# Kernel tuning notes

Hardware: AMD Instinct MI355X
Metric: run time of the kernel (lower is better)

## Reference

```python
import jax, jax.numpy as jnp
import numpy as np

D_MODEL = 1024
N_HEADS = 16
D_K = D_MODEL // N_HEADS
D_HIDDEN = 2048
LN_EPS = 1e-5


def setup_inputs() -> dict:
    key = jax.random.key(0)
    ks = jax.random.split(key, 16)
    s = 0.02
    inp = {
        'x': jax.random.normal(ks[0], (4, 2048, D_MODEL), dtype=jnp.float32),
        'Wq': jax.random.normal(ks[1], (D_MODEL, D_MODEL), dtype=jnp.float32) * s,
        'bq': jnp.zeros((D_MODEL,), jnp.float32),
        'Wk': jax.random.normal(ks[2], (D_MODEL, D_MODEL), dtype=jnp.float32) * s,
        'bk': jnp.zeros((D_MODEL,), jnp.float32),
        'Wv': jax.random.normal(ks[3], (D_MODEL, D_MODEL), dtype=jnp.float32) * s,
        'bv': jnp.zeros((D_MODEL,), jnp.float32),
        'Wo': jax.random.normal(ks[4], (D_MODEL, D_MODEL), dtype=jnp.float32) * s,
        'bo': jnp.zeros((D_MODEL,), jnp.float32),
        'ln1_g': jnp.ones((D_MODEL,), jnp.float32),
        'ln1_b': jnp.zeros((D_MODEL,), jnp.float32),
        'ln2_g': jnp.ones((D_MODEL,), jnp.float32),
        'ln2_b': jnp.zeros((D_MODEL,), jnp.float32),
        'W1': jax.random.normal(ks[5], (2 * D_HIDDEN, D_MODEL), dtype=jnp.float32) * s,
        'b1': jnp.zeros((2 * D_HIDDEN,), jnp.float32),
        'W2': jax.random.normal(ks[6], (D_MODEL, D_HIDDEN), dtype=jnp.float32) * s,
        'b2': jnp.zeros((D_MODEL,), jnp.float32),
    }
    return inp


def _layernorm(x, g, b):
    mu = jnp.mean(x, axis=-1, keepdims=True)
    var = jnp.mean(jnp.square(x - mu), axis=-1, keepdims=True)
    return (x - mu) * jax.lax.rsqrt(var + LN_EPS) * g + b


def _attention(xn, Wq, bq, Wk, bk, Wv, bv, Wo, bo):
    B, S, _ = xn.shape
    def split_heads(t):  # [B,S,D] -> [B,H,S,Dk]
        return t.reshape(B, S, N_HEADS, D_K).transpose(0, 2, 1, 3)
    Q = split_heads(xn @ Wq.T + bq)
    K = split_heads(xn @ Wk.T + bk)
    V = split_heads(xn @ Wv.T + bv)
    scores = jnp.einsum('bhqd,bhkd->bhqk', Q, K) / jnp.float32(D_K ** 0.5)
    attn = jax.nn.softmax(scores, axis=-1)  # torch code does max-sub + softmax (same math)
    ctx = jnp.einsum('bhqk,bhkd->bhqd', attn, V)
    ctx = ctx.transpose(0, 2, 1, 3).reshape(B, S, D_MODEL)
    return ctx @ Wo.T + bo


def reference(x, Wq, bq, Wk, bk, Wv, bv, Wo, bo, ln1_g, ln1_b, ln2_g, ln2_b, W1, b1, W2, b2):
    # pre-norm attention block
    xn = _layernorm(x, ln1_g, ln1_b)
    x = x + _attention(xn, Wq, bq, Wk, bk, Wv, bv, Wo, bo)
    # pre-norm ReGLU FFN
    xn = _layernorm(x, ln2_g, ln2_b)
    h = xn @ W1.T + b1
    a, b_ = jnp.split(h, 2, axis=-1)
    h = jax.nn.relu(a) * b_
    x = x + (h @ W2.T + b2)
    return x
```

## Files before the change

kernel.cpp:

```cpp
#include <hip/hip_runtime.h>
#include <hip/hip_bf16.h>

typedef __attribute__((ext_vector_type(8))) short short8;
typedef __attribute__((ext_vector_type(4))) float floatx4;

#define LN_EPS 1e-5f
#define EXP2_SCALE 0.18033688011112042f

__device__ __forceinline__ float b2f(unsigned short u) {
    union { float f; unsigned int i; } x; x.i = ((unsigned int)u) << 16; return x.f;
}
__device__ __forceinline__ unsigned short f2b(float f) {
    union { float f; unsigned int i; } x; x.f = f;
    unsigned int r = x.i + 0x7fffu + ((x.i >> 16) & 1u);
    return (unsigned short)(r >> 16);
}
__device__ __forceinline__ unsigned short f2b_trunc(float f) {
    union { float f; unsigned int i; } x; x.f = f;
    return (unsigned short)(x.i >> 16);
}

__device__ __forceinline__ void async16(const unsigned short* g, unsigned short* l) {
    __builtin_amdgcn_global_load_lds(
        (const __attribute__((address_space(1))) unsigned int*)g,
        (__attribute__((address_space(3))) unsigned int*)l, 16, 0, 0);
}

__global__ __launch_bounds__(256)
void cvt_all(const float* __restrict__ Wq, const float* __restrict__ Wk,
             const float* __restrict__ Wv, const float* __restrict__ Wo,
             const float* __restrict__ W1, const float* __restrict__ W2,
             unsigned short* __restrict__ dst)
{
    const size_t i = (size_t)(blockIdx.x * 256 + threadIdx.x) * 8;
    const float* src; size_t off;
    if (i < 4194304) {
        int w = (int)(i >> 20);
        src = (w == 0) ? Wq : (w == 1) ? Wk : (w == 2) ? Wv : Wo;
        off = i & 1048575;
    } else if (i < 8388608) { src = W1; off = i - 4194304; }
    else                    { src = W2; off = i - 8388608; }
    float4 a = *reinterpret_cast<const float4*>(src + off);
    float4 b = *reinterpret_cast<const float4*>(src + off + 4);
    short8 r;
    r[0] = (short)f2b(a.x); r[1] = (short)f2b(a.y);
    r[2] = (short)f2b(a.z); r[3] = (short)f2b(a.w);
    r[4] = (short)f2b(b.x); r[5] = (short)f2b(b.y);
    r[6] = (short)f2b(b.z); r[7] = (short)f2b(b.w);
    *reinterpret_cast<short8*>(dst + i) = r;
}

__global__ __launch_bounds__(256)
void ln_kernel(const float* __restrict__ x, const float* __restrict__ g,
               const float* __restrict__ bb, unsigned short* __restrict__ out)
{
    __shared__ float red[8];
    const int row = blockIdx.x, tid = threadIdx.x;
    const float* xr = x + (size_t)row * 1024;
    float v[4];
#pragma unroll
    for (int i = 0; i < 4; i++) v[i] = xr[tid + i * 256];
    float s  = v[0] + v[1] + v[2] + v[3];
    float sq = v[0]*v[0] + v[1]*v[1] + v[2]*v[2] + v[3]*v[3];
#pragma unroll
    for (int o = 32; o >= 1; o >>= 1) {
        s  += __shfl_xor(s,  o, 64);
        sq += __shfl_xor(sq, o, 64);
    }
    const int wave = tid >> 6, lane = tid & 63;
    if (lane == 0) { red[wave] = s; red[4 + wave] = sq; }
    __syncthreads();
    s  = red[0] + red[1] + red[2] + red[3];
    sq = red[4] + red[5] + red[6] + red[7];
    const float mu  = s * (1.0f / 1024.0f);
    const float var = sq * (1.0f / 1024.0f) - mu * mu;
    const float rs  = rsqrtf(var + LN_EPS);
#pragma unroll
    for (int i = 0; i < 4; i++) {
        int c = tid + i * 256;
        float o = (v[i] - mu) * rs * g[c] + bb[c];
        out[(size_t)row * 1024 + c] = f2b(o);
    }
}

struct GemmFrag {
    floatx4 acc[4][4];
};

template<int EPI>
__global__ __launch_bounds__(256, 2)
void gemm_nt(const unsigned short* __restrict__ A, const unsigned short* __restrict__ B,
             const float* __restrict__ bias, const float* __restrict__ res,
             void* __restrict__ C, int M, int N, int K)
{
    __shared__ unsigned short As[128 * 32];
    __shared__ unsigned short Bs[128 * 32];
    const int m0 = blockIdx.y * 128, n0 = blockIdx.x * 128;
    const int tid = threadIdx.x, wave = tid >> 6, lane = tid & 63;
    const int wm = (wave >> 1) * 64, wn = (wave & 1) * 64;
    const int lrow = lane & 15, quad = lane >> 4;
    const int srow = wave * 32 + (lane >> 2);
    const int scol = (lane & 3) * 8;

    floatx4 acc[4][4] = {};
    const unsigned short* gA = A + (size_t)(m0 + srow) * K + scol;
    const unsigned short* gB = B + (size_t)(n0 + srow) * K + scol;
    unsigned short* lA = &As[(wave * 32) * 32];
    unsigned short* lB = &Bs[(wave * 32) * 32];

    for (int k0 = 0; k0 < K; k0 += 32) {
        __syncthreads();
        async16(gA + k0, lA);
        async16(gA + k0 + (size_t)16 * K, lA + 16 * 32);
        async16(gB + k0, lB);
        async16(gB + k0 + (size_t)16 * K, lB + 16 * 32);
        __syncthreads();
        short8 af[4], bf[4];
#pragma unroll
        for (int i = 0; i < 4; i++)
            af[i] = *reinterpret_cast<const short8*>(&As[(wm + i * 16 + lrow) * 32 + quad * 8]);
#pragma unroll
        for (int j = 0; j < 4; j++)
            bf[j] = *reinterpret_cast<const short8*>(&Bs[(wn + j * 16 + lrow) * 32 + quad * 8]);
#pragma unroll
        for (int i = 0; i < 4; i++)
#pragma unroll
            for (int j = 0; j < 4; j++)
                acc[i][j] = __builtin_amdgcn_mfma_f32_16x16x32_bf16(af[i], bf[j], acc[i][j], 0, 0, 0);
    }

#pragma unroll
    for (int i = 0; i < 4; i++) {
        int rb = m0 + wm + i * 16 + quad * 4;
#pragma unroll
        for (int j = 0; j < 4; j++) {
            int col = n0 + wn + j * 16 + lrow;
            float bv = bias[col];
            if (EPI == 2) {
                int b = rb >> 11, spos = rb & 2047;
                int h = col >> 6, d = col & 63;
                unsigned short* dst = (unsigned short*)C +
                    (((size_t)(b * 16 + h) * 64 + d) << 11) + spos;
                unsigned int u01 = (unsigned int)f2b(acc[i][j][0] + bv) |
                                   ((unsigned int)f2b(acc[i][j][1] + bv) << 16);
                unsigned int u23 = (unsigned int)f2b(acc[i][j][2] + bv) |
                                   ((unsigned int)f2b(acc[i][j][3] + bv) << 16);
                *reinterpret_cast<uint2*>(dst) = make_uint2(u01, u23);
            } else {
#pragma unroll
                for (int r = 0; r < 4; r++) {
                    size_t idx = (size_t)(rb + r) * N + col;
                    float v = acc[i][j][r] + bv;
                    if (EPI == 0) ((unsigned short*)C)[idx] = f2b(v);
                    else          ((float*)C)[idx] = v + res[idx];
                }
            }
        }
    }
}

__global__ __launch_bounds__(256, 2)
void gemm_qkv(const unsigned short* __restrict__ A, const unsigned short* __restrict__ Wqkv,
              const float* __restrict__ bq, const float* __restrict__ bk, const float* __restrict__ bv,
              unsigned short* __restrict__ QK, unsigned short* __restrict__ Vt)
{
    __shared__ unsigned short As[128 * 32];
    __shared__ unsigned short Bs[128 * 32];
    const int part = blockIdx.x >> 3;
    const int m0 = blockIdx.y * 128, n0 = (blockIdx.x & 7) * 128;
    const int tid = threadIdx.x, wave = tid >> 6, lane = tid & 63;
    const int wm = (wave >> 1) * 64, wn = (wave & 1) * 64;
    const int lrow = lane & 15, quad = lane >> 4;
    const int srow = wave * 32 + (lane >> 2);
    const int scol = (lane & 3) * 8;
    const unsigned short* B = Wqkv + (size_t)part * 1048576;
    const float* bias = (part == 0) ? bq : (part == 1) ? bk : bv;

    floatx4 acc[4][4] = {};
    const unsigned short* gA = A + (size_t)(m0 + srow) * 1024 + scol;
    const unsigned short* gB = B + (size_t)(n0 + srow) * 1024 + scol;
    unsigned short* lA = &As[(wave * 32) * 32];
    unsigned short* lB = &Bs[(wave * 32) * 32];

    for (int k0 = 0; k0 < 1024; k0 += 32) {
        __syncthreads();
        async16(gA + k0, lA);
        async16(gA + k0 + (size_t)16 * 1024, lA + 16 * 32);
        async16(gB + k0, lB);
        async16(gB + k0 + (size_t)16 * 1024, lB + 16 * 32);
        __syncthreads();
        short8 af[4], bf[4];
#pragma unroll
        for (int i = 0; i < 4; i++)
            af[i] = *reinterpret_cast<const short8*>(&As[(wm + i * 16 + lrow) * 32 + quad * 8]);
#pragma unroll
        for (int j = 0; j < 4; j++)
            bf[j] = *reinterpret_cast<const short8*>(&Bs[(wn + j * 16 + lrow) * 32 + quad * 8]);
#pragma unroll
        for (int i = 0; i < 4; i++)
#pragma unroll
            for (int j = 0; j < 4; j++)
                acc[i][j] = __builtin_amdgcn_mfma_f32_16x16x32_bf16(af[i], bf[j], acc[i][j], 0, 0, 0);
    }

#pragma unroll
    for (int i = 0; i < 4; i++) {
        int rb = m0 + wm + i * 16 + quad * 4;
#pragma unroll
        for (int j = 0; j < 4; j++) {
            int col = n0 + wn + j * 16 + lrow;
            float bv2 = bias[col];
            if (part < 2) {
                unsigned short* dst = QK + (size_t)part * 8388608;
#pragma unroll
                for (int r = 0; r < 4; r++)
                    dst[(size_t)(rb + r) * 1024 + col] = f2b(acc[i][j][r] + bv2);
            } else {
                int b = rb >> 11, spos = rb & 2047;
                int h = col >> 6, d = col & 63;
                unsigned short* dst = Vt + (((size_t)(b * 16 + h) * 64 + d) << 11) + spos;
                unsigned int u01 = (unsigned int)f2b(acc[i][j][0] + bv2) |
                                   ((unsigned int)f2b(acc[i][j][1] + bv2) << 16);
                unsigned int u23 = (unsigned int)f2b(acc[i][j][2] + bv2) |
                                   ((unsigned int)f2b(acc[i][j][3] + bv2) << 16);
                *reinterpret_cast<uint2*>(dst) = make_uint2(u01, u23);
            }
        }
    }
}

__global__ __launch_bounds__(256, 2)
void gemm_w1_reglu(const unsigned short* __restrict__ A, const unsigned short* __restrict__ B,
                   const float* __restrict__ bias, unsigned short* __restrict__ G)
{
    __shared__ unsigned short As[128 * 32];
    __shared__ unsigned short B0s[128 * 32];
    __shared__ unsigned short B1s[128 * 32];
    const int m0 = blockIdx.y * 128, n0 = blockIdx.x * 128;
    const int tid = threadIdx.x, wave = tid >> 6, lane = tid & 63;
    const int wm = (wave >> 1) * 64, wn = (wave & 1) * 64;
    const int lrow = lane & 15, quad = lane >> 4;
    const int srow = wave * 32 + (lane >> 2);
    const int scol = (lane & 3) * 8;

    floatx4 acca[4][4] = {};
    floatx4 accb[4][4] = {};
    const unsigned short* gA  = A + (size_t)(m0 + srow) * 1024 + scol;
    const unsigned short* gB0 = B + (size_t)(n0 + srow) * 1024 + scol;
    const unsigned short* gB1 = B + (size_t)(2048 + n0 + srow) * 1024 + scol;
    unsigned short* lA  = &As [(wave * 32) * 32];
    unsigned short* lB0 = &B0s[(wave * 32) * 32];
    unsigned short* lB1 = &B1s[(wave * 32) * 32];

    for (int k0 = 0; k0 < 1024; k0 += 32) {
        __syncthreads();
        async16(gA  + k0, lA);
        async16(gA  + k0 + (size_t)16 * 1024, lA  + 16 * 32);
        async16(gB0 + k0, lB0);
        async16(gB0 + k0 + (size_t)16 * 1024, lB0 + 16 * 32);
        async16(gB1 + k0, lB1);
        async16(gB1 + k0 + (size_t)16 * 1024, lB1 + 16 * 32);
        __syncthreads();
        short8 af[4], b0[4], b1[4];
#pragma unroll
        for (int i = 0; i < 4; i++)
            af[i] = *reinterpret_cast<const short8*>(&As[(wm + i * 16 + lrow) * 32 + quad * 8]);
#pragma unroll
        for (int j = 0; j < 4; j++) {
            b0[j] = *reinterpret_cast<const short8*>(&B0s[(wn + j * 16 + lrow) * 32 + quad * 8]);
            b1[j] = *reinterpret_cast<const short8*>(&B1s[(wn + j * 16 + lrow) * 32 + quad * 8]);
        }
#pragma unroll
        for (int i = 0; i < 4; i++)
#pragma unroll
            for (int j = 0; j < 4; j++) {
                acca[i][j] = __builtin_amdgcn_mfma_f32_16x16x32_bf16(af[i], b0[j], acca[i][j], 0, 0, 0);
                accb[i][j] = __builtin_amdgcn_mfma_f32_16x16x32_bf16(af[i], b1[j], accb[i][j], 0, 0, 0);
            }
    }

#pragma unroll
    for (int i = 0; i < 4; i++) {
        int rb = m0 + wm + i * 16 + quad * 4;
#pragma unroll
        for (int j = 0; j < 4; j++) {
            int col = n0 + wn + j * 16 + lrow;
            float ba = bias[col], bb2 = bias[2048 + col];
#pragma unroll
            for (int r = 0; r < 4; r++) {
                float va = acca[i][j][r] + ba;
                float vb = accb[i][j][r] + bb2;
                G[(size_t)(rb + r) * 2048 + col] = f2b(fmaxf(va, 0.0f) * vb);
            }
        }
    }
}

__global__ __launch_bounds__(256, 2)
void attn_kernel(const unsigned short* __restrict__ Qm, const unsigned short* __restrict__ Km,
                 const unsigned short* __restrict__ Vt, unsigned short* __restrict__ ctx)
{
    __shared__ unsigned short Ks[64][72];
    __shared__ unsigned short Vs[64][72];
    __shared__ unsigned short Ps[4][32][72];

    const int tid = threadIdx.x, wave = tid >> 6, lane = tid & 63;
    const int lrow = lane & 15, quad = lane >> 4;
    const int qb = blockIdx.x, bh = blockIdx.y;
    const size_t base  = (size_t)(bh >> 4) * 2048 * 1024 + (size_t)(bh & 15) * 64;
    const size_t vbase = (size_t)bh * 131072;
    const int q0 = qb * 128 + wave * 32;

    short8 qf[2][2];
#pragma unroll
    for (int m = 0; m < 2; m++) {
        const unsigned short* qp = Qm + base + (size_t)(q0 + m * 16 + lrow) * 1024 + quad * 8;
        qf[m][0] = *reinterpret_cast<const short8*>(qp);
        qf[m][1] = *reinterpret_cast<const short8*>(qp + 32);
    }

    floatx4 o[2][4] = {};
    float li[2][4] = {};

    const int c0 = tid, c1 = tid + 256;
    for (int t = 0; t < 32; t++) {
        const int k0 = t * 64;
        __syncthreads();
        {
            int r0 = c0 >> 3, col0 = (c0 & 7) << 3;
            int r1 = c1 >> 3, col1 = (c1 & 7) << 3;
            *reinterpret_cast<uint4*>(&Ks[r0][col0]) =
                *reinterpret_cast<const uint4*>(Km + base + (size_t)(k0 + r0) * 1024 + col0);
            *reinterpret_cast<uint4*>(&Ks[r1][col1]) =
                *reinterpret_cast<const uint4*>(Km + base + (size_t)(k0 + r1) * 1024 + col1);
            *reinterpret_cast<uint4*>(&Vs[r0][col0]) =
                *reinterpret_cast<const uint4*>(Vt + vbase + (size_t)r0 * 2048 + k0 + col0);
            *reinterpret_cast<uint4*>(&Vs[r1][col1]) =
                *reinterpret_cast<const uint4*>(Vt + vbase + (size_t)r1 * 2048 + k0 + col1);
        }
        __syncthreads();

        short8 kf0[4], kf1[4];
#pragma unroll
        for (int j = 0; j < 4; j++) {
            kf0[j] = *reinterpret_cast<const short8*>(&Ks[j * 16 + lrow][quad * 8]);
            kf1[j] = *reinterpret_cast<const short8*>(&Ks[j * 16 + lrow][32 + quad * 8]);
        }
        floatx4 s4[2][4] = {};
#pragma unroll
        for (int m = 0; m < 2; m++)
#pragma unroll
            for (int j = 0; j < 4; j++) {
                s4[m][j] = __builtin_amdgcn_mfma_f32_16x16x32_bf16(qf[m][0], kf0[j], s4[m][j], 0, 0, 0);
                s4[m][j] = __builtin_amdgcn_mfma_f32_16x16x32_bf16(qf[m][1], kf1[j], s4[m][j], 0, 0, 0);
            }

#pragma unroll
        for (int m = 0; m < 2; m++)
#pragma unroll
            for (int r = 0; r < 4; r++) {
                float acc = 0.f;
#pragma unroll
                for (int j = 0; j < 4; j++) {
                    float p = __builtin_amdgcn_exp2f(s4[m][j][r] * EXP2_SCALE);
                    acc += p;
                    Ps[wave][m * 16 + quad * 4 + r][j * 16 + lrow] = f2b_trunc(p);
                }
                li[m][r] += acc;
            }
        __asm__ volatile("s_waitcnt lgkmcnt(0)" ::: "memory");

        short8 pf[2][2];
#pragma unroll
        for (int m = 0; m < 2; m++) {
            pf[m][0] = *reinterpret_cast<const short8*>(&Ps[wave][m * 16 + lrow][quad * 8]);
            pf[m][1] = *reinterpret_cast<const short8*>(&Ps[wave][m * 16 + lrow][32 + quad * 8]);
        }
#pragma unroll
        for (int jj = 0; jj < 4; jj++) {
            short8 vf0 = *reinterpret_cast<const short8*>(&Vs[jj * 16 + lrow][quad * 8]);
            short8 vf1 = *reinterpret_cast<const short8*>(&Vs[jj * 16 + lrow][32 + quad * 8]);
#pragma unroll
            for (int m = 0; m < 2; m++) {
                o[m][jj] = __builtin_amdgcn_mfma_f32_16x16x32_bf16(pf[m][0], vf0, o[m][jj], 0, 0, 0);
                o[m][jj] = __builtin_amdgcn_mfma_f32_16x16x32_bf16(pf[m][1], vf1, o[m][jj], 0, 0, 0);
            }
        }
    }

#pragma unroll
    for (int m = 0; m < 2; m++)
#pragma unroll
        for (int r = 0; r < 4; r++) {
            float l = li[m][r];
            l += __shfl_xor(l, 1, 64);
            l += __shfl_xor(l, 2, 64);
            l += __shfl_xor(l, 4, 64);
            l += __shfl_xor(l, 8, 64);
            float inv = 1.0f / l;
            int srow = q0 + m * 16 + quad * 4 + r;
#pragma unroll
            for (int jj = 0; jj < 4; jj++)
                ctx[base + (size_t)srow * 1024 + jj * 16 + lrow] = f2b(o[m][jj][r] * inv);
        }
}

extern "C" void kernel_launch(void* const* d_in, const int* in_sizes, int n_in,
                              void* d_out, int out_size, void* d_ws, size_t ws_size,
                              hipStream_t stream) {
    const float* x    = (const float*)d_in[0];
    const float* Wq   = (const float*)d_in[1];
    const float* bq   = (const float*)d_in[2];
    const float* Wk   = (const float*)d_in[3];
    const float* bk   = (const float*)d_in[4];
    const float* Wv   = (const float*)d_in[5];
    const float* bv   = (const float*)d_in[6];
    const float* Wo   = (const float*)d_in[7];
    const float* bo   = (const float*)d_in[8];
    const float* ln1g = (const float*)d_in[9];
    const float* ln1b = (const float*)d_in[10];
    const float* ln2g = (const float*)d_in[11];
    const float* ln2b = (const float*)d_in[12];
    const float* W1   = (const float*)d_in[13];
    const float* b1   = (const float*)d_in[14];
    const float* W2   = (const float*)d_in[15];
    const float* b2   = (const float*)d_in[16];
    float* out = (float*)d_out;

    char* ws = (char*)d_ws;
    unsigned short* wflat = (unsigned short*)ws;
    unsigned short* wqb = wflat;
    unsigned short* wob = wflat + 3145728;
    unsigned short* w1b = wflat + 4194304;
    unsigned short* w2b = wflat + 8388608;
    unsigned short* xn  = (unsigned short*)(ws + 20971520);
    unsigned short* Qm  = (unsigned short*)(ws + 37748736);
    unsigned short* Vt  = (unsigned short*)(ws + 71303168);
    float*          x1  = (float*)(ws + 37748736);
    unsigned short* g   = (unsigned short*)(ws + 71303168);

    dim3 blk(256);
    cvt_all<<<5120, blk, 0, stream>>>(Wq, Wk, Wv, Wo, W1, W2, wflat);
    ln_kernel<<<8192, blk, 0, stream>>>(x, ln1g, ln1b, xn);
    gemm_qkv<<<dim3(24, 64), blk, 0, stream>>>(xn, wqb, bq, bk, bv, Qm, Vt);
    attn_kernel<<<dim3(16, 64), blk, 0, stream>>>(Qm, Qm + 8388608, Vt, xn);
    gemm_nt<1><<<dim3(8, 64), blk, 0, stream>>>(xn, wob, bo, x, x1, 8192, 1024, 1024);
    ln_kernel<<<8192, blk, 0, stream>>>(x1, ln2g, ln2b, xn);
    gemm_w1_reglu<<<dim3(16, 64), blk, 0, stream>>>(xn, w1b, b1, g);
    gemm_nt<1><<<dim3(8, 64), blk, 0, stream>>>(g, w2b, b2, x1, out, 8192, 1024, 2048);
}
```

Baseline: 494.9 us.

## Widen GEMM K-tile to 64 with XOR-swizzled LDS and async attention loads

All GEMM kernels now stage 64-wide K slices in LDS, with an XOR swizzle on both the global-to-LDS copy and the fragment reads, halving the number of barrier pairs per K loop and avoiding bank conflicts. The attention kernel switches its K/V staging from register round-trip copies to direct global-to-LDS async loads using the same swizzle. The softmax exp2 scale is folded into the Q projection epilogue, which removes a multiply per score. Launch bounds are raised to 3 blocks per CU, at the cost of doubled LDS per block and tighter register limits that could cause spills.

```diff
diff --git a/kernel.cpp b/kernel.cpp
--- a/kernel.cpp
+++ b/kernel.cpp
@@ -83,45 +83,55 @@
     }
 }
 
-struct GemmFrag {
-    floatx4 acc[4][4];
-};
-
 template<int EPI>
-__global__ __launch_bounds__(256, 2)
+__global__ __launch_bounds__(256, 3)
 void gemm_nt(const unsigned short* __restrict__ A, const unsigned short* __restrict__ B,
              const float* __restrict__ bias, const float* __restrict__ res,
              void* __restrict__ C, int M, int N, int K)
 {
-    __shared__ unsigned short As[128 * 32];
-    __shared__ unsigned short Bs[128 * 32];
+    __shared__ unsigned short As[128 * 64];
+    __shared__ unsigned short Bs[128 * 64];
     const int m0 = blockIdx.y * 128, n0 = blockIdx.x * 128;
     const int tid = threadIdx.x, wave = tid >> 6, lane = tid & 63;
     const int wm = (wave >> 1) * 64, wn = (wave & 1) * 64;
     const int lrow = lane & 15, quad = lane >> 4;
-    const int srow = wave * 32 + (lane >> 2);
-    const int scol = (lane & 3) * 8;
+    const int srow = wave * 32 + (lane >> 3);
+    const int scol = (((lane & 7) ^ ((lane >> 3) & 7)) << 3);
+    const int ca0 = (quad ^ (lrow & 7)) << 3;
+    const int ca1 = ((quad + 4) ^ (lrow & 7)) << 3;
 
     floatx4 acc[4][4] = {};
     const unsigned short* gA = A + (size_t)(m0 + srow) * K + scol;
     const unsigned short* gB = B + (size_t)(n0 + srow) * K + scol;
-    unsigned short* lA = &As[(wave * 32) * 32];
-    unsigned short* lB = &Bs[(wave * 32) * 32];
-
-    for (int k0 = 0; k0 < K; k0 += 32) {
-        __syncthreads();
-        async16(gA + k0, lA);
-        async16(gA + k0 + (size_t)16 * K, lA + 16 * 32);
-        async16(gB + k0, lB);
-        async16(gB + k0 + (size_t)16 * K, lB + 16 * 32);
+    unsigned short* lA = &As[(wave * 32) * 64];
+    unsigned short* lB = &Bs[(wave * 32) * 64];
+
+    for (int k0 = 0; k0 < K; k0 += 64) {
+        __syncthreads();
+#pragma unroll
+        for (int r = 0; r < 4; r++) {
+            async16(gA + k0 + (size_t)(r * 8) * K, lA + r * 8 * 64);
+            async16(gB + k0 + (size_t)(r * 8) * K, lB + r * 8 * 64);
+        }
         __syncthreads();
         short8 af[4], bf[4];
 #pragma unroll
         for (int i = 0; i < 4; i++)
-            af[i] = *reinterpret_cast<const short8*>(&As[(wm + i * 16 + lrow) * 32 + quad * 8]);
+            af[i] = *reinterpret_cast<const short8*>(&As[(wm + i * 16 + lrow) * 64 + ca0]);
 #pragma unroll
         for (int j = 0; j < 4; j++)
-            bf[j] = *reinterpret_cast<const short8*>(&Bs[(wn + j * 16 + lrow) * 32 + quad * 8]);
+            bf[j] = *reinterpret_cast<const short8*>(&Bs[(wn + j * 16 + lrow) * 64 + ca0]);
+#pragma unroll
+        for (int i = 0; i < 4; i++)
+#pragma unroll
+            for (int j = 0; j < 4; j++)
+                acc[i][j] = __builtin_amdgcn_mfma_f32_16x16x32_bf16(af[i], bf[j], acc[i][j], 0, 0, 0);
+#pragma unroll
+        for (int i = 0; i < 4; i++)
+            af[i] = *reinterpret_cast<const short8*>(&As[(wm + i * 16 + lrow) * 64 + ca1]);
+#pragma unroll
+        for (int j = 0; j < 4; j++)
+            bf[j] = *reinterpret_cast<const short8*>(&Bs[(wn + j * 16 + lrow) * 64 + ca1]);
 #pragma unroll
         for (int i = 0; i < 4; i++)
 #pragma unroll
@@ -136,66 +146,68 @@
         for (int j = 0; j < 4; j++) {
             int col = n0 + wn + j * 16 + lrow;
             float bv = bias[col];
-            if (EPI == 2) {
-                int b = rb >> 11, spos = rb & 2047;
-                int h = col >> 6, d = col & 63;
-                unsigned short* dst = (unsigned short*)C +
-                    (((size_t)(b * 16 + h) * 64 + d) << 11) + spos;
-                unsigned int u01 = (unsigned int)f2b(acc[i][j][0] + bv) |
-                                   ((unsigned int)f2b(acc[i][j][1] + bv) << 16);
-                unsigned int u23 = (unsigned int)f2b(acc[i][j][2] + bv) |
-                                   ((unsigned int)f2b(acc[i][j][3] + bv) << 16);
-                *reinterpret_cast<uint2*>(dst) = make_uint2(u01, u23);
-            } else {
-#pragma unroll
-                for (int r = 0; r < 4; r++) {
-                    size_t idx = (size_t)(rb + r) * N + col;
-                    float v = acc[i][j][r] + bv;
-                    if (EPI == 0) ((unsigned short*)C)[idx] = f2b(v);
-                    else          ((float*)C)[idx] = v + res[idx];
-                }
-            }
-        }
-    }
-}
-
-__global__ __launch_bounds__(256, 2)
+#pragma unroll
+            for (int r = 0; r < 4; r++) {
+                size_t idx = (size_t)(rb + r) * N + col;
+                float v = acc[i][j][r] + bv;
+                if (EPI == 0) ((unsigned short*)C)[idx] = f2b(v);
+                else          ((float*)C)[idx] = v + res[idx];
+            }
+        }
+    }
+}
+
+__global__ __launch_bounds__(256, 3)
 void gemm_qkv(const unsigned short* __restrict__ A, const unsigned short* __restrict__ Wqkv,
               const float* __restrict__ bq, const float* __restrict__ bk, const float* __restrict__ bv,
               unsigned short* __restrict__ QK, unsigned short* __restrict__ Vt)
 {
-    __shared__ unsigned short As[128 * 32];
-    __shared__ unsigned short Bs[128 * 32];
+    __shared__ unsigned short As[128 * 64];
+    __shared__ unsigned short Bs[128 * 64];
     const int part = blockIdx.x >> 3;
     const int m0 = blockIdx.y * 128, n0 = (blockIdx.x & 7) * 128;
     const int tid = threadIdx.x, wave = tid >> 6, lane = tid & 63;
     const int wm = (wave >> 1) * 64, wn = (wave & 1) * 64;
     const int lrow = lane & 15, quad = lane >> 4;
-    const int srow = wave * 32 + (lane >> 2);
-    const int scol = (lane & 3) * 8;
+    const int srow = wave * 32 + (lane >> 3);
+    const int scol = (((lane & 7) ^ ((lane >> 3) & 7)) << 3);
+    const int ca0 = (quad ^ (lrow & 7)) << 3;
+    const int ca1 = ((quad + 4) ^ (lrow & 7)) << 3;
     const unsigned short* B = Wqkv + (size_t)part * 1048576;
     const float* bias = (part == 0) ? bq : (part == 1) ? bk : bv;
 
     floatx4 acc[4][4] = {};
     const unsigned short* gA = A + (size_t)(m0 + srow) * 1024 + scol;
     const unsigned short* gB = B + (size_t)(n0 + srow) * 1024 + scol;
-    unsigned short* lA = &As[(wave * 32) * 32];
-    unsigned short* lB = &Bs[(wave * 32) * 32];
-
-    for (int k0 = 0; k0 < 1024; k0 += 32) {
-        __syncthreads();
-        async16(gA + k0, lA);
-        async16(gA + k0 + (size_t)16 * 1024, lA + 16 * 32);
-        async16(gB + k0, lB);
-        async16(gB + k0 + (size_t)16 * 1024, lB + 16 * 32);
+    unsigned short* lA = &As[(wave * 32) * 64];
+    unsigned short* lB = &Bs[(wave * 32) * 64];
+
+    for (int k0 = 0; k0 < 1024; k0 += 64) {
+        __syncthreads();
+#pragma unroll
+        for (int r = 0; r < 4; r++) {
+            async16(gA + k0 + (size_t)(r * 8) * 1024, lA + r * 8 * 64);
+            async16(gB + k0 + (size_t)(r * 8) * 1024, lB + r * 8 * 64);
+        }
         __syncthreads();
         short8 af[4], bf[4];
 #pragma unroll
         for (int i = 0; i < 4; i++)
-            af[i] = *reinterpret_cast<const short8*>(&As[(wm + i * 16 + lrow) * 32 + quad * 8]);
+            af[i] = *reinterpret_cast<const short8*>(&As[(wm + i * 16 + lrow) * 64 + ca0]);
 #pragma unroll
         for (int j = 0; j < 4; j++)
-            bf[j] = *reinterpret_cast<const short8*>(&Bs[(wn + j * 16 + lrow) * 32 + quad * 8]);
+            bf[j] = *reinterpret_cast<const short8*>(&Bs[(wn + j * 16 + lrow) * 64 + ca0]);
+#pragma unroll
+        for (int i = 0; i < 4; i++)
+#pragma unroll
+            for (int j = 0; j < 4; j++)
+                acc[i][j] = __builtin_amdgcn_mfma_f32_16x16x32_bf16(af[i], bf[j], acc[i][j], 0, 0, 0);
+#pragma unroll
+        for (int i = 0; i < 4; i++)
+            af[i] = *reinterpret_cast<const short8*>(&As[(wm + i * 16 + lrow) * 64 + ca1]);
+#pragma unroll
+        for (int j = 0; j < 4; j++)
+            bf[j] = *reinterpret_cast<const short8*>(&Bs[(wn + j * 16 + lrow) * 64 + ca1]);
 #pragma unroll
         for (int i = 0; i < 4; i++)
 #pragma unroll
@@ -210,8 +222,12 @@
         for (int j = 0; j < 4; j++) {
             int col = n0 + wn + j * 16 + lrow;
             float bv2 = bias[col];
-            if (part < 2) {
-                unsigned short* dst = QK + (size_t)part * 8388608;
+            if (part == 0) {
+#pragma unroll
+                for (int r = 0; r < 4; r++)
+                    QK[(size_t)(rb + r) * 1024 + col] = f2b((acc[i][j][r] + bv2) * EXP2_SCALE);
+            } else if (part == 1) {
+                unsigned short* dst = QK + 8388608;
 #pragma unroll
                 for (int r = 0; r < 4; r++)
                     dst[(size_t)(rb + r) * 1024 + col] = f2b(acc[i][j][r] + bv2);
@@ -233,50 +249,56 @@
 void gemm_w1_reglu(const unsigned short* __restrict__ A, const unsigned short* __restrict__ B,
                    const float* __restrict__ bias, unsigned short* __restrict__ G)
 {
-    __shared__ unsigned short As[128 * 32];
-    __shared__ unsigned short B0s[128 * 32];
-    __shared__ unsigned short B1s[128 * 32];
+    __shared__ unsigned short As[128 * 64];
+    __shared__ unsigned short B0s[128 * 64];
+    __shared__ unsigned short B1s[128 * 64];
     const int m0 = blockIdx.y * 128, n0 = blockIdx.x * 128;
     const int tid = threadIdx.x, wave = tid >> 6, lane = tid & 63;
     const int wm = (wave >> 1) * 64, wn = (wave & 1) * 64;
     const int lrow = lane & 15, quad = lane >> 4;
-    const int srow = wave * 32 + (lane >> 2);
-    const int scol = (lane & 3) * 8;
+    const int srow = wave * 32 + (lane >> 3);
+    const int scol = (((lane & 7) ^ ((lane >> 3) & 7)) << 3);
+    const int ca0 = (quad ^ (lrow & 7)) << 3;
+    const int ca1 = ((quad + 4) ^ (lrow & 7)) << 3;
 
     floatx4 acca[4][4] = {};
     floatx4 accb[4][4] = {};
     const unsigned short* gA  = A + (size_t)(m0 + srow) * 1024 + scol;
     const unsigned short* gB0 = B + (size_t)(n0 + srow) * 1024 + scol;
     const unsigned short* gB1 = B + (size_t)(2048 + n0 + srow) * 1024 + scol;
-    unsigned short* lA  = &As [(wave * 32) * 32];
-    unsigned short* lB0 = &B0s[(wave * 32) * 32];
-    unsigned short* lB1 = &B1s[(wave * 32) * 32];
-
-    for (int k0 = 0; k0 < 1024; k0 += 32) {
-        __syncthreads();
-        async16(gA  + k0, lA);
-        async16(gA  + k0 + (size_t)16 * 1024, lA  + 16 * 32);
-        async16(gB0 + k0, lB0);
-        async16(gB0 + k0 + (size_t)16 * 1024, lB0 + 16 * 32);
-        async16(gB1 + k0, lB1);
-        async16(gB1 + k0 + (size_t)16 * 1024, lB1 + 16 * 32);
-        __syncthreads();
-        short8 af[4], b0[4], b1[4];
-#pragma unroll
-        for (int i = 0; i < 4; i++)
-            af[i] = *reinterpret_cast<const short8*>(&As[(wm + i * 16 + lrow) * 32 + quad * 8]);
-#pragma unroll
-        for (int j = 0; j < 4; j++) {
-            b0[j] = *reinterpret_cast<const short8*>(&B0s[(wn + j * 16 + lrow) * 32 + quad * 8]);
-            b1[j] = *reinterpret_cast<const short8*>(&B1s[(wn + j * 16 + lrow) * 32 + quad * 8]);
-        }
-#pragma unroll
-        for (int i = 0; i < 4; i++)
+    unsigned short* lA  = &As [(wave * 32) * 64];
+    unsigned short* lB0 = &B0s[(wave * 32) * 64];
+    unsigned short* lB1 = &B1s[(wave * 32) * 64];
+
+    for (int k0 = 0; k0 < 1024; k0 += 64) {
+        __syncthreads();
+#pragma unroll
+        for (int r = 0; r < 4; r++) {
+            async16(gA  + k0 + (size_t)(r * 8) * 1024, lA  + r * 8 * 64);
+            async16(gB0 + k0 + (size_t)(r * 8) * 1024, lB0 + r * 8 * 64);
+            async16(gB1 + k0 + (size_t)(r * 8) * 1024, lB1 + r * 8 * 64);
+        }
+        __syncthreads();
+#pragma unroll
+        for (int ks = 0; ks < 2; ks++) {
+            const int ca = ks ? ca1 : ca0;
+            short8 af[4], b0[4], b1[4];
+#pragma unroll
+            for (int i = 0; i < 4; i++)
+                af[i] = *reinterpret_cast<const short8*>(&As[(wm + i * 16 + lrow) * 64 + ca]);
 #pragma unroll
             for (int j = 0; j < 4; j++) {
-                acca[i][j] = __builtin_amdgcn_mfma_f32_16x16x32_bf16(af[i], b0[j], acca[i][j], 0, 0, 0);
-                accb[i][j] = __builtin_amdgcn_mfma_f32_16x16x32_bf16(af[i], b1[j], accb[i][j], 0, 0, 0);
-            }
+                b0[j] = *reinterpret_cast<const short8*>(&B0s[(wn + j * 16 + lrow) * 64 + ca]);
+                b1[j] = *reinterpret_cast<const short8*>(&B1s[(wn + j * 16 + lrow) * 64 + ca]);
+            }
+#pragma unroll
+            for (int i = 0; i < 4; i++)
+#pragma unroll
+                for (int j = 0; j < 4; j++) {
+                    acca[i][j] = __builtin_amdgcn_mfma_f32_16x16x32_bf16(af[i], b0[j], acca[i][j], 0, 0, 0);
+                    accb[i][j] = __builtin_amdgcn_mfma_f32_16x16x32_bf16(af[i], b1[j], accb[i][j], 0, 0, 0);
+                }
+        }
     }
 
 #pragma unroll
@@ -296,12 +318,12 @@
     }
 }
 
-__global__ __launch_bounds__(256, 2)
+__global__ __launch_bounds__(256, 3)
 void attn_kernel(const unsigned short* __restrict__ Qm, const unsigned short* __restrict__ Km,
                  const unsigned short* __restrict__ Vt, unsigned short* __restrict__ ctx)
 {
-    __shared__ unsigned short Ks[64][72];
-    __shared__ unsigned short Vs[64][72];
+    __shared__ unsigned short Ks[64 * 64];
+    __shared__ unsigned short Vs[64 * 64];
     __shared__ unsigned short Ps[4][32][72];
 
     const int tid = threadIdx.x, wave = tid >> 6, lane = tid & 63;
@@ -310,6 +332,10 @@
     const size_t base  = (size_t)(bh >> 4) * 2048 * 1024 + (size_t)(bh & 15) * 64;
     const size_t vbase = (size_t)bh * 131072;
     const int q0 = qb * 128 + wave * 32;
+    const int g_sub = (lane >> 3);
+    const int g_col = (((lane & 7) ^ (g_sub & 7)) << 3);
+    const int ca0 = (quad ^ (lrow & 7)) << 3;
+    const int ca1 = ((quad + 4) ^ (lrow & 7)) << 3;
 
     short8 qf[2][2];
 #pragma unroll
@@ -322,29 +348,22 @@
     floatx4 o[2][4] = {};
     float li[2][4] = {};
 
-    const int c0 = tid, c1 = tid + 256;
     for (int t = 0; t < 32; t++) {
         const int k0 = t * 64;
         __syncthreads();
-        {
-            int r0 = c0 >> 3, col0 = (c0 & 7) << 3;
-            int r1 = c1 >> 3, col1 = (c1 & 7) << 3;
-            *reinterpret_cast<uint4*>(&Ks[r0][col0]) =
-                *reinterpret_cast<const uint4*>(Km + base + (size_t)(k0 + r0) * 1024 + col0);
-            *reinterpret_cast<uint4*>(&Ks[r1][col1]) =
-                *reinterpret_cast<const uint4*>(Km + base + (size_t)(k0 + r1) * 1024 + col1);
-            *reinterpret_cast<uint4*>(&Vs[r0][col0]) =
-                *reinterpret_cast<const uint4*>(Vt + vbase + (size_t)r0 * 2048 + k0 + col0);
-            *reinterpret_cast<uint4*>(&Vs[r1][col1]) =
-                *reinterpret_cast<const uint4*>(Vt + vbase + (size_t)r1 * 2048 + k0 + col1);
+#pragma unroll
+        for (int r = 0; r < 2; r++) {
+            int krow = wave * 16 + r * 8 + g_sub;
+            async16(Km + base + (size_t)(k0 + krow) * 1024 + g_col, &Ks[(wave * 16 + r * 8) * 64]);
+            async16(Vt + vbase + (size_t)krow * 2048 + k0 + g_col,  &Vs[(wave * 16 + r * 8) * 64]);
         }
         __syncthreads();
 
         short8 kf0[4], kf1[4];
 #pragma unroll
         for (int j = 0; j < 4; j++) {
-            kf0[j] = *reinterpret_cast<const short8*>(&Ks[j * 16 + lrow][quad * 8]);
-            kf1[j] = *reinterpret_cast<const short8*>(&Ks[j * 16 + lrow][32 + quad * 8]);
+            kf0[j] = *reinterpret_cast<const short8*>(&Ks[(j * 16 + lrow) * 64 + ca0]);
+            kf1[j] = *reinterpret_cast<const short8*>(&Ks[(j * 16 + lrow) * 64 + ca1]);
         }
         floatx4 s4[2][4] = {};
 #pragma unroll
@@ -362,7 +381,7 @@
                 float acc = 0.f;
 #pragma unroll
                 for (int j = 0; j < 4; j++) {
-                    float p = __builtin_amdgcn_exp2f(s4[m][j][r] * EXP2_SCALE);
+                    float p = __builtin_amdgcn_exp2f(s4[m][j][r]);
                     acc += p;
                     Ps[wave][m * 16 + quad * 4 + r][j * 16 + lrow] = f2b_trunc(p);
                 }
@@ -378,8 +397,8 @@
         }
 #pragma unroll
         for (int jj = 0; jj < 4; jj++) {
-            short8 vf0 = *reinterpret_cast<const short8*>(&Vs[jj * 16 + lrow][quad * 8]);
-            short8 vf1 = *reinterpret_cast<const short8*>(&Vs[jj * 16 + lrow][32 + quad * 8]);
+            short8 vf0 = *reinterpret_cast<const short8*>(&Vs[(jj * 16 + lrow) * 64 + ca0]);
+            short8 vf1 = *reinterpret_cast<const short8*>(&Vs[(jj * 16 + lrow) * 64 + ca1]);
 #pragma unroll
             for (int m = 0; m < 2; m++) {
                 o[m][jj] = __builtin_amdgcn_mfma_f32_16x16x32_bf16(pf[m][0], vf0, o[m][jj], 0, 0, 0);
```

Result: faster. 452.7 us (-8.5%).
